# Performance work log

Measured on AMD Instinct MI355X. Metric: run time of the kernel, lower is better.

The kernel has to match this reference:

```python
import jax, jax.numpy as jnp
import numpy as np

R = 131072  # rays
S = 128     # samples per ray
LAMBDA_OPACITY = 1e-3
LAMBDA_DISTORTION = 1e-3


def setup_inputs() -> dict:
    key = jax.random.key(0)
    ks = jax.random.split(key, 5)
    rgb_pred = jax.random.uniform(ks[0], (R, 3), dtype=jnp.float32)
    rgb_gt = jax.random.uniform(ks[1], (R, 3), dtype=jnp.float32)
    opacity = jax.random.uniform(ks[2], (R, 1), dtype=jnp.float32, minval=1e-3, maxval=1.0)
    ws = jax.random.uniform(ks[3], (R * S,), dtype=jnp.float32) / S  # sample weights, sum<=1 per ray
    deltas = jax.random.uniform(ks[4], (R * S,), dtype=jnp.float32) * 0.02 + 1e-4  # interval lengths
    # midpoints must be sorted ascending within each ray (kernel assumption)
    ts = (jnp.cumsum(deltas.reshape(R, S), axis=1) + 0.1).reshape(-1)
    # rays_a: (ray_idx, start_idx, N_samples) -- uniform S samples per ray
    rays_a = jnp.stack([jnp.arange(R), jnp.arange(R) * S, jnp.full((R,), S)], axis=1).astype(jnp.int32)
    return {"rgb_pred": rgb_pred, "rgb_gt": rgb_gt, "opacity": opacity,
            "ws": ws, "deltas": deltas, "ts": ts, "rays_a": rays_a}


def distortion_loss(ws, deltas, ts, rays_a):
    """Mip-NeRF-360 distortion loss (DVGO-v2 prefix-scan form), per ray.
    rays_a encodes contiguous, uniform-length segments (S samples/ray)."""
    n_rays = rays_a.shape[0]
    s = ws.shape[0] // n_rays
    w = ws.reshape(n_rays, s)
    t = ts.reshape(n_rays, s)
    d = deltas.reshape(n_rays, s)
    wt = w * t
    cw = jnp.cumsum(w, axis=1) - w     # exclusive inclusive-scan of w
    cwt = jnp.cumsum(wt, axis=1) - wt  # exclusive inclusive-scan of w*t
    # sum_{i>j} 2 w_i w_j (t_i - t_j)  +  (1/3) sum_i w_i^2 delta_i
    loss_bi = 2.0 * jnp.sum(w * (t * cw - cwt), axis=1)
    loss_uni = jnp.sum(w * w * d, axis=1) / 3.0
    return loss_bi + loss_uni  # (n_rays,)


def reference(rgb_pred, rgb_gt, opacity, ws, deltas, ts, rays_a):
    rgb_loss = (rgb_pred - rgb_gt) ** 2                      # (R,3)
    o = opacity + 1e-10
    opacity_loss = LAMBDA_OPACITY * (-o * jnp.log(o))        # (R,1)
    dist_loss = LAMBDA_DISTORTION * distortion_loss(ws, deltas, ts, rays_a)  # (R,)
    return (rgb_loss, opacity_loss, dist_loss)
```

## Files before the change

### kernel.cpp

```cpp
#include <hip/hip_runtime.h>
#include <math.h>


constexpr float K_LAMBDA_OPACITY = 1e-3f;
constexpr float K_LAMBDA_DISTORTION = 1e-3f;
constexpr int K_S = 128;

__global__ __launch_bounds__(256) void nerf_loss_kernel(
    const float* __restrict__ rgb_pred,
    const float* __restrict__ rgb_gt,
    const float* __restrict__ opacity,
    const float* __restrict__ ws,
    const float* __restrict__ deltas,
    const float* __restrict__ ts,
    float* __restrict__ out,
    int R)
{
    const int lane = threadIdx.x & 63;
    const int ray  = (blockIdx.x * blockDim.x + threadIdx.x) >> 6;
    if (ray >= R) return;

    const int base = ray * K_S + lane * 2;
    const float2 w2 = *(const float2*)(ws + base);
    const float2 t2 = *(const float2*)(ts + base);
    const float2 d2 = *(const float2*)(deltas + base);

    const float wt0 = w2.x * t2.x;
    const float wt1 = w2.y * t2.y;
    float inc_w  = w2.x + w2.y;
    float inc_wt = wt0 + wt1;
    const float sw  = inc_w;
    const float swt = inc_wt;

    #pragma unroll
    for (int off = 1; off < 64; off <<= 1) {
        float yw  = __shfl_up(inc_w,  off, 64);
        float ywt = __shfl_up(inc_wt, off, 64);
        if (lane >= off) { inc_w += yw; inc_wt += ywt; }
    }
    float cw  = inc_w  - sw;
    float cwt = inc_wt - swt;

    float bi = w2.x * (t2.x * cw - cwt);
    cw  += w2.x;
    cwt += wt0;
    bi  += w2.y * (t2.y * cw - cwt);

    const float uni = w2.x * w2.x * d2.x + w2.y * w2.y * d2.y;
    float part = 2.0f * bi + uni * (1.0f / 3.0f);

    #pragma unroll
    for (int off = 32; off > 0; off >>= 1)
        part += __shfl_down(part, off, 64);

    if (lane == 0)
        out[(size_t)R * 4 + ray] = K_LAMBDA_DISTORTION * part;

    if (lane < 3) {
        const int idx = ray * 3 + lane;
        const float diff = rgb_pred[idx] - rgb_gt[idx];
        out[idx] = diff * diff;
    } else if (lane == 3) {
        const float o = opacity[ray] + 1e-10f;
        out[(size_t)R * 3 + ray] = K_LAMBDA_OPACITY * (-o * logf(o));
    }
}

extern "C" void kernel_launch(void* const* d_in, const int* in_sizes, int n_in,
                              void* d_out, int out_size, void* d_ws, size_t ws_size,
                              hipStream_t stream) {
    const float* rgb_pred = (const float*)d_in[0];
    const float* rgb_gt   = (const float*)d_in[1];
    const float* opacity  = (const float*)d_in[2];
    const float* ws       = (const float*)d_in[3];
    const float* deltas   = (const float*)d_in[4];
    const float* ts       = (const float*)d_in[5];
    float* out = (float*)d_out;

    const int R = in_sizes[0] / 3;
    const int rays_per_block = 256 / 64;
    const int blocks = (R + rays_per_block - 1) / rays_per_block;

    nerf_loss_kernel<<<blocks, 256, 0, stream>>>(
        rgb_pred, rgb_gt, opacity, ws, deltas, ts, out, R);
}
```

Measured before the change: 201.7 us.

## Process four rays per wave with 8 samples per lane and segmented scans

Each lane now loads 8 consecutive samples as two float4 loads per array and does a sequential local scan, so one wavefront handles four rays in 16-lane segments. The cross-lane prefix scan and reduction shrink from 6 to 4 shuffle steps, and the carried-in prefix is applied algebraically to the local partial sums. This cuts shuffle and instruction overhead per sample and widens memory accesses, at the cost of more registers per thread and a quarter as many waves. Partial final waves are not guarded when R is not a multiple of 4.

```diff
diff --git a/kernel.cpp b/kernel.cpp
--- a/kernel.cpp
+++ b/kernel.cpp
@@ -5,6 +5,8 @@
 constexpr float K_LAMBDA_OPACITY = 1e-3f;
 constexpr float K_LAMBDA_DISTORTION = 1e-3f;
 constexpr int K_S = 128;
+constexpr int K_SPL = 8;
+constexpr int K_RAYS_PER_WAVE = 4;
 
 __global__ __launch_bounds__(256) void nerf_loss_kernel(
     const float* __restrict__ rgb_pred,
@@ -17,50 +19,63 @@
     int R)
 {
     const int lane = threadIdx.x & 63;
-    const int ray  = (blockIdx.x * blockDim.x + threadIdx.x) >> 6;
-    if (ray >= R) return;
+    const int wave = (blockIdx.x * blockDim.x + threadIdx.x) >> 6;
+    const int ray_base = wave * K_RAYS_PER_WAVE;
+    if (ray_base >= R) return;
 
-    const int base = ray * K_S + lane * 2;
-    const float2 w2 = *(const float2*)(ws + base);
-    const float2 t2 = *(const float2*)(ts + base);
-    const float2 d2 = *(const float2*)(deltas + base);
+    const size_t base = (size_t)wave * (64 * K_SPL) + (size_t)lane * K_SPL;
+    const float4 w0 = *(const float4*)(ws + base);
+    const float4 w1 = *(const float4*)(ws + base + 4);
+    const float4 t0 = *(const float4*)(ts + base);
+    const float4 t1 = *(const float4*)(ts + base + 4);
+    const float4 d0 = *(const float4*)(deltas + base);
+    const float4 d1 = *(const float4*)(deltas + base + 4);
 
-    const float wt0 = w2.x * t2.x;
-    const float wt1 = w2.y * t2.y;
-    float inc_w  = w2.x + w2.y;
-    float inc_wt = wt0 + wt1;
-    const float sw  = inc_w;
-    const float swt = inc_wt;
+    float cw = 0.f, cwt = 0.f, bi = 0.f, uni = 0.f;
+    const float w[K_SPL] = {w0.x, w0.y, w0.z, w0.w, w1.x, w1.y, w1.z, w1.w};
+    const float t[K_SPL] = {t0.x, t0.y, t0.z, t0.w, t1.x, t1.y, t1.z, t1.w};
+    const float d[K_SPL] = {d0.x, d0.y, d0.z, d0.w, d1.x, d1.y, d1.z, d1.w};
+    #pragma unroll
+    for (int j = 0; j < K_SPL; ++j) {
+        const float wt = w[j] * t[j];
+        bi  += w[j] * (t[j] * cw - cwt);
+        uni += w[j] * w[j] * d[j];
+        cw  += w[j];
+        cwt += wt;
+    }
+    const float sw_local  = cw;
+    const float swt_local = cwt;
 
+    float inc_w = sw_local, inc_wt = swt_local;
+    const int seg_lane = lane & 15;
     #pragma unroll
-    for (int off = 1; off < 64; off <<= 1) {
-        float yw  = __shfl_up(inc_w,  off, 64);
-        float ywt = __shfl_up(inc_wt, off, 64);
-        if (lane >= off) { inc_w += yw; inc_wt += ywt; }
+    for (int off = 1; off < 16; off <<= 1) {
+        const float yw  = __shfl_up(inc_w,  off, 64);
+        const float ywt = __shfl_up(inc_wt, off, 64);
+        if (seg_lane >= off) { inc_w += yw; inc_wt += ywt; }
     }
-    float cw  = inc_w  - sw;
-    float cwt = inc_wt - swt;
+    const float cw_base  = inc_w  - sw_local;
+    const float cwt_base = inc_wt - swt_local;
 
-    float bi = w2.x * (t2.x * cw - cwt);
-    cw  += w2.x;
-    cwt += wt0;
-    bi  += w2.y * (t2.y * cw - cwt);
+    bi += cw_base * swt_local - cwt_base * sw_local;
 
-    const float uni = w2.x * w2.x * d2.x + w2.y * w2.y * d2.y;
     float part = 2.0f * bi + uni * (1.0f / 3.0f);
 
     #pragma unroll
-    for (int off = 32; off > 0; off >>= 1)
-        part += __shfl_down(part, off, 64);
+    for (int off = 1; off < 16; off <<= 1)
+        part += __shfl_xor(part, off, 64);
 
-    if (lane == 0)
+    if (seg_lane == 0) {
+        const int ray = ray_base + (lane >> 4);
         out[(size_t)R * 4 + ray] = K_LAMBDA_DISTORTION * part;
+    }
 
-    if (lane < 3) {
-        const int idx = ray * 3 + lane;
+    if (lane < 12) {
+        const int idx = wave * 12 + lane;
         const float diff = rgb_pred[idx] - rgb_gt[idx];
         out[idx] = diff * diff;
-    } else if (lane == 3) {
+    } else if (lane < 16) {
+        const int ray = ray_base + (lane - 12);
         const float o = opacity[ray] + 1e-10f;
         out[(size_t)R * 3 + ray] = K_LAMBDA_OPACITY * (-o * logf(o));
     }
@@ -78,7 +93,7 @@
     float* out = (float*)d_out;
 
     const int R = in_sizes[0] / 3;
-    const int rays_per_block = 256 / 64;
+    const int rays_per_block = (256 / 64) * K_RAYS_PER_WAVE;
     const int blocks = (R + rays_per_block - 1) / rays_per_block;
 
     nerf_loss_kernel<<<blocks, 256, 0, stream>>>(
```

New measurement: 204.3 us. No clear change (+1.3%).
